# Optimization experiments

Hardware: AMD Instinct MI355X
Metric: run time of the kernel (lower is better)

The kernel has to match this reference:

```python
import jax, jax.numpy as jnp
import numpy as np

N_NODES = 100000

def gcn_conv(x, W, b, src, dst, n_nodes):
    # PyG GCNConv: out = D^{-1/2} (A + I) D^{-1/2} (x W) + b, deg includes self-loop
    h = x @ W  # [N, H]
    ones = jnp.ones(src.shape[0], dtype=x.dtype)
    deg = jax.ops.segment_sum(ones, dst, num_segments=n_nodes) + 1.0  # +1 self-loop
    dinv = jax.lax.rsqrt(deg)  # deg >= 1, no zeros
    norm = dinv[src] * dinv[dst]  # [E]
    msg = h[src] * norm[:, None]  # [E, H] gather + scale
    agg = jax.ops.segment_sum(msg, dst, num_segments=n_nodes)  # scatter-add
    self_contrib = h * (dinv * dinv)[:, None]  # self-loop term norm = dinv_i^2
    return agg + self_contrib + b


def setup_inputs() -> dict:
    key = jax.random.key(0)
    ks = jax.random.split(key, 6)
    F_IN, H, E = 128, 128, 1600000
    x = jax.random.normal(ks[0], (N_NODES, F_IN), dtype=jnp.float32)
    edge_index = jax.random.randint(ks[1], (2, E), 0, N_NODES, dtype=jnp.int32)
    s = 1.0 / np.sqrt(F_IN)
    W1 = jax.random.normal(ks[2], (F_IN, H), dtype=jnp.float32) * s
    b1 = jnp.zeros((H,), dtype=jnp.float32)
    W2 = jax.random.normal(ks[3], (H, H), dtype=jnp.float32) * (1.0 / np.sqrt(H))
    b2 = jnp.zeros((H,), dtype=jnp.float32)
    Wlin = jax.random.normal(ks[4], (H, 1), dtype=jnp.float32) * (1.0 / np.sqrt(H))
    blin = jnp.zeros((1,), dtype=jnp.float32)
    return {"x": x, "edge_index": edge_index, "W1": W1, "b1": b1,
            "W2": W2, "b2": b2, "Wlin": Wlin, "blin": blin}


def reference(x, edge_index, W1, b1, W2, b2, Wlin, blin):
    src, dst = edge_index[0], edge_index[1]
    h = gcn_conv(x, W1, b1, src, dst, N_NODES)
    h = jax.nn.relu(h)
    h = gcn_conv(h, W2, b2, src, dst, N_NODES)
    h = jax.nn.relu(h)
    out = h @ Wlin + blin  # [N, 1]
    return out.squeeze(-1)  # [N]
```

## Files before the change

kernel.cpp:

```cpp
#include <hip/hip_runtime.h>
#include <hip/hip_fp16.h>

#define NFEAT 128

typedef _Float16 v8hf __attribute__((ext_vector_type(8)));
typedef float v4f __attribute__((ext_vector_type(4)));

__global__ void k_deg_rank(const int* __restrict__ dst, int* __restrict__ deg,
                           int* __restrict__ rank, int E, int N) {
  int e = blockIdx.x * blockDim.x + threadIdx.x;
  if (e < E) rank[e] = atomicAdd(&deg[dst[e]], 1);
  else if (e < E + N) rank[e] = atomicAdd(&deg[e - E], 1);
}

__global__ void k_prep_w(const float* __restrict__ W1, const float* __restrict__ W2,
                         _Float16* __restrict__ Wt1, _Float16* __restrict__ Wt2) {
  int idx = blockIdx.x * 256 + threadIdx.x;
  const float* W = (idx < 16384) ? W1 : W2;
  _Float16* Wt = (idx < 16384) ? Wt1 : Wt2;
  int i = idx & 16383;
  int k = i >> 7, n = i & 127;
  Wt[n * 128 + k] = (_Float16)W[k * 128 + n];
}

__global__ __launch_bounds__(1024) void k_scan_blocks(const int* __restrict__ deg,
    int* __restrict__ base, int* __restrict__ partials, int n) {
  __shared__ int buf[1024];
  int tid = threadIdx.x;
  int i = blockIdx.x * 1024 + tid;
  int v = (i < n) ? deg[i] : 0;
  buf[tid] = v;
  __syncthreads();
  #pragma unroll
  for (int off = 1; off < 1024; off <<= 1) {
    int t = (tid >= off) ? buf[tid - off] : 0;
    __syncthreads();
    buf[tid] += t;
    __syncthreads();
  }
  if (i <= n) base[i] = buf[tid] - v;
  if (tid == 1023) partials[blockIdx.x] = buf[tid];
}

__global__ void k_scan_partials(int* __restrict__ partials, int nb) {
  __shared__ int buf[128];
  int tid = threadIdx.x;
  int v = (tid < nb) ? partials[tid] : 0;
  buf[tid] = v;
  __syncthreads();
  #pragma unroll
  for (int off = 1; off < 128; off <<= 1) {
    int t = (tid >= off) ? buf[tid - off] : 0;
    __syncthreads();
    buf[tid] += t;
    __syncthreads();
  }
  if (tid < nb) partials[tid] = buf[tid] - v;
}

__global__ void k_finalize_base(int* __restrict__ base, const int* __restrict__ partials,
    const int* __restrict__ deg, float* __restrict__ dinv, int n) {
  int i = blockIdx.x * blockDim.x + threadIdx.x;
  if (i <= n) {
    base[i] += partials[i >> 10];
    if (i < n) dinv[i] = rsqrtf((float)deg[i]);
  }
}

__global__ void k_scatter(const int* __restrict__ src, const int* __restrict__ dst,
    const int* __restrict__ rank, const int* __restrict__ base,
    int* __restrict__ ssrc, int E, int N) {
  int e = blockIdx.x * blockDim.x + threadIdx.x;
  if (e < E) ssrc[base[dst[e]] + rank[e]] = src[e];
  else if (e < E + N) { int n = e - E; ssrc[base[n] + rank[e]] = n; }
}

template <typename AT>
__global__ __launch_bounds__(256) void k_gemm_mfma(
    const AT* __restrict__ A, const _Float16* __restrict__ Wt,
    const float* __restrict__ dinv, _Float16* __restrict__ g16, int N) {
  __shared__ _Float16 As[64][136];
  __shared__ _Float16 Ws[128][136];
  const int tid = threadIdx.x;
  const int row0 = blockIdx.x * 64;

  if constexpr (sizeof(AT) == 4) {
    #pragma unroll
    for (int i = 0; i < 8; i++) {
      int idx = tid + i * 256;
      int row = idx >> 5;
      int c4 = idx & 31;
      int gr = row0 + row; gr = (gr < N) ? gr : (N - 1);
      float4 v = *(const float4*)((const float*)A + (size_t)gr * NFEAT + c4 * 4);
      _Float16* p = &As[row][c4 * 4];
      p[0] = (_Float16)v.x; p[1] = (_Float16)v.y;
      p[2] = (_Float16)v.z; p[3] = (_Float16)v.w;
    }
  } else {
    #pragma unroll
    for (int i = 0; i < 4; i++) {
      int idx = tid + i * 256;
      int row = idx >> 4;
      int c8 = idx & 15;
      int gr = row0 + row; gr = (gr < N) ? gr : (N - 1);
      *(uint4*)&As[row][c8 * 8] =
          *(const uint4*)((const _Float16*)A + (size_t)gr * NFEAT + c8 * 8);
    }
  }
  #pragma unroll
  for (int i = 0; i < 8; i++) {
    int idx = tid + i * 256;
    int row = idx >> 4;
    int c8 = idx & 15;
    *(uint4*)&Ws[row][c8 * 8] = *(const uint4*)(Wt + (size_t)row * 128 + c8 * 8);
  }
  __syncthreads();

  const int wv = tid >> 6;
  const int lane = tid & 63;
  const int m = lane & 15;
  const int q = lane >> 4;

  v4f acc[8] = {};
  const _Float16* arow = &As[wv * 16 + m][0];
  #pragma unroll
  for (int kt = 0; kt < 4; kt++) {
    v8hf af = *(const v8hf*)(arow + kt * 32 + q * 8);
    #pragma unroll
    for (int ct = 0; ct < 8; ct++) {
      v8hf bf = *(const v8hf*)(&Ws[ct * 16 + m][kt * 32 + q * 8]);
      acc[ct] = __builtin_amdgcn_mfma_f32_16x16x32_f16(af, bf, acc[ct], 0, 0, 0);
    }
  }

  int nd[4]; float dv[4];
  #pragma unroll
  for (int r = 0; r < 4; r++) {
    nd[r] = row0 + wv * 16 + q * 4 + r;
    int c = (nd[r] < N) ? nd[r] : (N - 1);
    dv[r] = dinv[c];
  }
  #pragma unroll
  for (int ct = 0; ct < 8; ct++)
    #pragma unroll
    for (int r = 0; r < 4; r++)
      if (nd[r] < N)
        g16[(size_t)nd[r] * NFEAT + ct * 16 + m] = (_Float16)(acc[ct][r] * dv[r]);
}

__global__ __launch_bounds__(256) void k_agg(
    const __half2* __restrict__ g, const float* __restrict__ dinv,
    const int* __restrict__ base, const int* __restrict__ ssrc,
    const float* __restrict__ bias, __half2* __restrict__ hB, int N) {
  const int lane = threadIdx.x & 63;
  const int n = blockIdx.x * 4 + (threadIdx.x >> 6);
  if (n >= N) return;
  int e = base[n], b1 = base[n + 1];
  float2 acc = make_float2(0.f, 0.f);
  for (; e + 8 <= b1; e += 8) {
    int s0 = ssrc[e],     s1 = ssrc[e + 1], s2 = ssrc[e + 2], s3 = ssrc[e + 3];
    int s4 = ssrc[e + 4], s5 = ssrc[e + 5], s6 = ssrc[e + 6], s7 = ssrc[e + 7];
    float2 f0 = __half22float2(g[(size_t)s0 * 64 + lane]);
    float2 f1 = __half22float2(g[(size_t)s1 * 64 + lane]);
    float2 f2 = __half22float2(g[(size_t)s2 * 64 + lane]);
    float2 f3 = __half22float2(g[(size_t)s3 * 64 + lane]);
    float2 f4 = __half22float2(g[(size_t)s4 * 64 + lane]);
    float2 f5 = __half22float2(g[(size_t)s5 * 64 + lane]);
    float2 f6 = __half22float2(g[(size_t)s6 * 64 + lane]);
    float2 f7 = __half22float2(g[(size_t)s7 * 64 + lane]);
    acc.x += (f0.x + f1.x) + (f2.x + f3.x) + (f4.x + f5.x) + (f6.x + f7.x);
    acc.y += (f0.y + f1.y) + (f2.y + f3.y) + (f4.y + f5.y) + (f6.y + f7.y);
  }
  for (; e < b1; ++e) {
    float2 f = __half22float2(g[(size_t)ssrc[e] * 64 + lane]);
    acc.x += f.x; acc.y += f.y;
  }
  float dvn = dinv[n];
  float2 bb = *(const float2*)(bias + lane * 2);
  hB[(size_t)n * 64 + lane] =
      __floats2half2_rn(fmaxf(acc.x * dvn + bb.x, 0.f),
                        fmaxf(acc.y * dvn + bb.y, 0.f));
}

__global__ __launch_bounds__(256) void k_agg_final(
    const __half2* __restrict__ g, const float* __restrict__ dinv,
    const int* __restrict__ base, const int* __restrict__ ssrc,
    const float* __restrict__ bias, const float* __restrict__ wlin,
    const float* __restrict__ blin, float* __restrict__ out, int N) {
  const int lane = threadIdx.x & 63;
  const int n = blockIdx.x * 4 + (threadIdx.x >> 6);
  if (n >= N) return;
  int e = base[n], b1 = base[n + 1];
  float2 acc = make_float2(0.f, 0.f);
  for (; e + 8 <= b1; e += 8) {
    int s0 = ssrc[e],     s1 = ssrc[e + 1], s2 = ssrc[e + 2], s3 = ssrc[e + 3];
    int s4 = ssrc[e + 4], s5 = ssrc[e + 5], s6 = ssrc[e + 6], s7 = ssrc[e + 7];
    float2 f0 = __half22float2(g[(size_t)s0 * 64 + lane]);
    float2 f1 = __half22float2(g[(size_t)s1 * 64 + lane]);
    float2 f2 = __half22float2(g[(size_t)s2 * 64 + lane]);
    float2 f3 = __half22float2(g[(size_t)s3 * 64 + lane]);
    float2 f4 = __half22float2(g[(size_t)s4 * 64 + lane]);
    float2 f5 = __half22float2(g[(size_t)s5 * 64 + lane]);
    float2 f6 = __half22float2(g[(size_t)s6 * 64 + lane]);
    float2 f7 = __half22float2(g[(size_t)s7 * 64 + lane]);
    acc.x += (f0.x + f1.x) + (f2.x + f3.x) + (f4.x + f5.x) + (f6.x + f7.x);
    acc.y += (f0.y + f1.y) + (f2.y + f3.y) + (f4.y + f5.y) + (f6.y + f7.y);
  }
  for (; e < b1; ++e) {
    float2 f = __half22float2(g[(size_t)ssrc[e] * 64 + lane]);
    acc.x += f.x; acc.y += f.y;
  }
  float dvn = dinv[n];
  float2 bb = *(const float2*)(bias + lane * 2);
  float2 wl = *(const float2*)(wlin + lane * 2);
  float pv = fmaxf(acc.x * dvn + bb.x, 0.f) * wl.x +
             fmaxf(acc.y * dvn + bb.y, 0.f) * wl.y;
  #pragma unroll
  for (int off = 32; off >= 1; off >>= 1) pv += __shfl_down(pv, off, 64);
  if (lane == 0) out[n] = pv + blin[0];
}

extern "C" void kernel_launch(void* const* d_in, const int* in_sizes, int n_in,
                              void* d_out, int out_size, void* d_ws, size_t ws_size,
                              hipStream_t stream) {
  const float* x    = (const float*)d_in[0];
  const int*   ei   = (const int*)d_in[1];
  const float* W1   = (const float*)d_in[2];
  const float* b1   = (const float*)d_in[3];
  const float* W2   = (const float*)d_in[4];
  const float* b2   = (const float*)d_in[5];
  const float* Wlin = (const float*)d_in[6];
  const float* blin = (const float*)d_in[7];
  const int N = in_sizes[0] / NFEAT;
  const int E = in_sizes[1] / 2;
  const int* src = ei;
  const int* dst = ei + E;
  const int Etot = E + N;

  int* ws_i = (int*)d_ws;
  size_t off = 0;
  int* deg      = ws_i + off; off += N;
  int* base     = ws_i + off; off += (size_t)N + 1;
  off = (off + 3) & ~(size_t)3;
  int* partials = ws_i + off; off += 128;
  int* ssrc     = ws_i + off; off += Etot;
  float* dinv   = (float*)(ws_i + off); off += N;
  off = (off + 3) & ~(size_t)3;
  _Float16* Wt1 = (_Float16*)(ws_i + off); off += 8192;
  _Float16* Wt2 = (_Float16*)(ws_i + off); off += 8192;
  _Float16* g16 = (_Float16*)(ws_i + off); off += (size_t)N * 64;
  _Float16* hB  = (_Float16*)(ws_i + off); off += (size_t)N * 64;
  int* rank     = (int*)g16;

  hipMemsetAsync(deg, 0, (size_t)N * sizeof(int), stream);

  const int tpbE = 256;
  const int gE = (Etot + tpbE - 1) / tpbE;
  k_deg_rank<<<gE, tpbE, 0, stream>>>(dst, deg, rank, E, N);
  k_prep_w<<<128, 256, 0, stream>>>(W1, W2, Wt1, Wt2);

  const int nb = (N + 1 + 1023) / 1024;
  k_scan_blocks<<<nb, 1024, 0, stream>>>(deg, base, partials, N);
  k_scan_partials<<<1, 128, 0, stream>>>(partials, nb);
  k_finalize_base<<<((N + 1) + 255) / 256, 256, 0, stream>>>(base, partials, deg, dinv, N);
  k_scatter<<<gE, tpbE, 0, stream>>>(src, dst, rank, base, ssrc, E, N);

  const int gg = (N + 63) / 64;
  const int ga = (N + 3) / 4;
  k_gemm_mfma<float><<<gg, 256, 0, stream>>>(x, Wt1, dinv, g16, N);
  k_agg<<<ga, 256, 0, stream>>>((const __half2*)g16, dinv, base, ssrc, b1,
                                (__half2*)hB, N);
  k_gemm_mfma<_Float16><<<gg, 256, 0, stream>>>(hB, Wt2, dinv, g16, N);
  k_agg_final<<<ga, 256, 0, stream>>>((const __half2*)g16, dinv, base, ssrc, b2,
                                      Wlin, blin, (float*)d_out, N);
}
```

Measured before the change: 401.2 us.

## Split wavefront into four edge groups with 16-byte vector gathers in aggregation

The aggregation kernels now split each 64-lane wavefront into four 16-lane groups. Each group gathers a whole 256-byte fp16 row with 16-byte vector loads, so one wave handles eight edges per iteration and partial sums are combined with cross-lane shuffles. Out-of-range edges are pointed at a zero padding row appended to the feature buffer, which removes the scalar tail loop. The weight-transpose kernel is also merged into the degree/rank kernel to save a launch. The cost is the extra shuffle reductions and some wasted loads on padded edges for low-degree nodes.

```diff
diff --git a/kernel.cpp b/kernel.cpp
--- a/kernel.cpp
+++ b/kernel.cpp
@@ -6,21 +6,21 @@
 typedef _Float16 v8hf __attribute__((ext_vector_type(8)));
 typedef float v4f __attribute__((ext_vector_type(4)));
 
-__global__ void k_deg_rank(const int* __restrict__ dst, int* __restrict__ deg,
-                           int* __restrict__ rank, int E, int N) {
+__global__ void k_deg_rank_w(const int* __restrict__ dst, int* __restrict__ deg,
+                             int* __restrict__ rank, int E, int N,
+                             const float* __restrict__ W1, const float* __restrict__ W2,
+                             _Float16* __restrict__ Wt1, _Float16* __restrict__ Wt2) {
   int e = blockIdx.x * blockDim.x + threadIdx.x;
   if (e < E) rank[e] = atomicAdd(&deg[dst[e]], 1);
   else if (e < E + N) rank[e] = atomicAdd(&deg[e - E], 1);
-}
-
-__global__ void k_prep_w(const float* __restrict__ W1, const float* __restrict__ W2,
-                         _Float16* __restrict__ Wt1, _Float16* __restrict__ Wt2) {
-  int idx = blockIdx.x * 256 + threadIdx.x;
-  const float* W = (idx < 16384) ? W1 : W2;
-  _Float16* Wt = (idx < 16384) ? Wt1 : Wt2;
-  int i = idx & 16383;
-  int k = i >> 7, n = i & 127;
-  Wt[n * 128 + k] = (_Float16)W[k * 128 + n];
+  else if (e < E + N + 32768) {
+    int idx = e - E - N;
+    const float* W = (idx < 16384) ? W1 : W2;
+    _Float16* Wt = (idx < 16384) ? Wt1 : Wt2;
+    int i = idx & 16383;
+    int k = i >> 7, n = i & 127;
+    Wt[n * 128 + k] = (_Float16)W[k * 128 + n];
+  }
 }
 
 __global__ __launch_bounds__(1024) void k_scan_blocks(const int* __restrict__ deg,
@@ -83,6 +83,13 @@
   __shared__ _Float16 Ws[128][136];
   const int tid = threadIdx.x;
   const int row0 = blockIdx.x * 64;
+
+  if (blockIdx.x == 0 && tid < 16) {
+    v8hf z;
+    #pragma unroll
+    for (int j = 0; j < 8; j++) z[j] = (_Float16)0.f;
+    *(v8hf*)(g16 + (size_t)N * NFEAT + tid * 8) = z;
+  }
 
   if constexpr (sizeof(AT) == 4) {
     #pragma unroll
@@ -149,74 +156,91 @@
 }
 
 __global__ __launch_bounds__(256) void k_agg(
-    const __half2* __restrict__ g, const float* __restrict__ dinv,
+    const _Float16* __restrict__ g, const float* __restrict__ dinv,
     const int* __restrict__ base, const int* __restrict__ ssrc,
-    const float* __restrict__ bias, __half2* __restrict__ hB, int N) {
+    const float* __restrict__ bias, _Float16* __restrict__ hB, int N) {
   const int lane = threadIdx.x & 63;
   const int n = blockIdx.x * 4 + (threadIdx.x >> 6);
   if (n >= N) return;
-  int e = base[n], b1 = base[n + 1];
-  float2 acc = make_float2(0.f, 0.f);
-  for (; e + 8 <= b1; e += 8) {
-    int s0 = ssrc[e],     s1 = ssrc[e + 1], s2 = ssrc[e + 2], s3 = ssrc[e + 3];
-    int s4 = ssrc[e + 4], s5 = ssrc[e + 5], s6 = ssrc[e + 6], s7 = ssrc[e + 7];
-    float2 f0 = __half22float2(g[(size_t)s0 * 64 + lane]);
-    float2 f1 = __half22float2(g[(size_t)s1 * 64 + lane]);
-    float2 f2 = __half22float2(g[(size_t)s2 * 64 + lane]);
-    float2 f3 = __half22float2(g[(size_t)s3 * 64 + lane]);
-    float2 f4 = __half22float2(g[(size_t)s4 * 64 + lane]);
-    float2 f5 = __half22float2(g[(size_t)s5 * 64 + lane]);
-    float2 f6 = __half22float2(g[(size_t)s6 * 64 + lane]);
-    float2 f7 = __half22float2(g[(size_t)s7 * 64 + lane]);
-    acc.x += (f0.x + f1.x) + (f2.x + f3.x) + (f4.x + f5.x) + (f6.x + f7.x);
-    acc.y += (f0.y + f1.y) + (f2.y + f3.y) + (f4.y + f5.y) + (f6.y + f7.y);
-  }
-  for (; e < b1; ++e) {
-    float2 f = __half22float2(g[(size_t)ssrc[e] * 64 + lane]);
-    acc.x += f.x; acc.y += f.y;
-  }
-  float dvn = dinv[n];
-  float2 bb = *(const float2*)(bias + lane * 2);
-  hB[(size_t)n * 64 + lane] =
-      __floats2half2_rn(fmaxf(acc.x * dvn + bb.x, 0.f),
-                        fmaxf(acc.y * dvn + bb.y, 0.f));
+  const int gq = lane >> 4;
+  const int l = lane & 15;
+  float acc[8] = {};
+  int b0 = base[n], b1 = base[n + 1];
+  for (int e = b0; e < b1; e += 8) {
+    int e0 = e + gq, e1 = e + 4 + gq;
+    int i0 = ssrc[e0];
+    int i1 = ssrc[e1];
+    i0 = (e0 < b1) ? i0 : N;
+    i1 = (e1 < b1) ? i1 : N;
+    v8hf r0 = *(const v8hf*)(g + (size_t)i0 * NFEAT + l * 8);
+    v8hf r1 = *(const v8hf*)(g + (size_t)i1 * NFEAT + l * 8);
+    #pragma unroll
+    for (int j = 0; j < 8; j++) acc[j] += (float)r0[j] + (float)r1[j];
+  }
+  #pragma unroll
+  for (int j = 0; j < 8; j++) {
+    acc[j] += __shfl_xor(acc[j], 16, 64);
+    acc[j] += __shfl_xor(acc[j], 32, 64);
+  }
+  if (gq == 0) {
+    float dvn = dinv[n];
+    const float* bp = bias + l * 8;
+    float4 bb0 = *(const float4*)(bp);
+    float4 bb1 = *(const float4*)(bp + 4);
+    float bv[8] = {bb0.x, bb0.y, bb0.z, bb0.w, bb1.x, bb1.y, bb1.z, bb1.w};
+    v8hf o;
+    #pragma unroll
+    for (int j = 0; j < 8; j++)
+      o[j] = (_Float16)fmaxf(acc[j] * dvn + bv[j], 0.f);
+    *(v8hf*)(hB + (size_t)n * NFEAT + l * 8) = o;
+  }
 }
 
 __global__ __launch_bounds__(256) void k_agg_final(
-    const __half2* __restrict__ g, const float* __restrict__ dinv,
+    const _Float16* __restrict__ g, const float* __restrict__ dinv,
     const int* __restrict__ base, const int* __restrict__ ssrc,
     const float* __restrict__ bias, const float* __restrict__ wlin,
     const float* __restrict__ blin, float* __restrict__ out, int N) {
   const int lane = threadIdx.x & 63;
   const int n = blockIdx.x * 4 + (threadIdx.x >> 6);
   if (n >= N) return;
-  int e = base[n], b1 = base[n + 1];
-  float2 acc = make_float2(0.f, 0.f);
-  for (; e + 8 <= b1; e += 8) {
-    int s0 = ssrc[e],     s1 = ssrc[e + 1], s2 = ssrc[e + 2], s3 = ssrc[e + 3];
-    int s4 = ssrc[e + 4], s5 = ssrc[e + 5], s6 = ssrc[e + 6], s7 = ssrc[e + 7];
-    float2 f0 = __half22float2(g[(size_t)s0 * 64 + lane]);
-    float2 f1 = __half22float2(g[(size_t)s1 * 64 + lane]);
-    float2 f2 = __half22float2(g[(size_t)s2 * 64 + lane]);
-    float2 f3 = __half22float2(g[(size_t)s3 * 64 + lane]);
-    float2 f4 = __half22float2(g[(size_t)s4 * 64 + lane]);
-    float2 f5 = __half22float2(g[(size_t)s5 * 64 + lane]);
-    float2 f6 = __half22float2(g[(size_t)s6 * 64 + lane]);
-    float2 f7 = __half22float2(g[(size_t)s7 * 64 + lane]);
-    acc.x += (f0.x + f1.x) + (f2.x + f3.x) + (f4.x + f5.x) + (f6.x + f7.x);
-    acc.y += (f0.y + f1.y) + (f2.y + f3.y) + (f4.y + f5.y) + (f6.y + f7.y);
-  }
-  for (; e < b1; ++e) {
-    float2 f = __half22float2(g[(size_t)ssrc[e] * 64 + lane]);
-    acc.x += f.x; acc.y += f.y;
+  const int gq = lane >> 4;
+  const int l = lane & 15;
+  float acc[8] = {};
+  int b0 = base[n], b1 = base[n + 1];
+  for (int e = b0; e < b1; e += 8) {
+    int e0 = e + gq, e1 = e + 4 + gq;
+    int i0 = ssrc[e0];
+    int i1 = ssrc[e1];
+    i0 = (e0 < b1) ? i0 : N;
+    i1 = (e1 < b1) ? i1 : N;
+    v8hf r0 = *(const v8hf*)(g + (size_t)i0 * NFEAT + l * 8);
+    v8hf r1 = *(const v8hf*)(g + (size_t)i1 * NFEAT + l * 8);
+    #pragma unroll
+    for (int j = 0; j < 8; j++) acc[j] += (float)r0[j] + (float)r1[j];
+  }
+  #pragma unroll
+  for (int j = 0; j < 8; j++) {
+    acc[j] += __shfl_xor(acc[j], 16, 64);
+    acc[j] += __shfl_xor(acc[j], 32, 64);
   }
   float dvn = dinv[n];
-  float2 bb = *(const float2*)(bias + lane * 2);
-  float2 wl = *(const float2*)(wlin + lane * 2);
-  float pv = fmaxf(acc.x * dvn + bb.x, 0.f) * wl.x +
-             fmaxf(acc.y * dvn + bb.y, 0.f) * wl.y;
-  #pragma unroll
-  for (int off = 32; off >= 1; off >>= 1) pv += __shfl_down(pv, off, 64);
+  const float* bp = bias + l * 8;
+  const float* wp = wlin + l * 8;
+  float4 bb0 = *(const float4*)(bp);
+  float4 bb1 = *(const float4*)(bp + 4);
+  float4 wl0 = *(const float4*)(wp);
+  float4 wl1 = *(const float4*)(wp + 4);
+  float bv[8] = {bb0.x, bb0.y, bb0.z, bb0.w, bb1.x, bb1.y, bb1.z, bb1.w};
+  float wv[8] = {wl0.x, wl0.y, wl0.z, wl0.w, wl1.x, wl1.y, wl1.z, wl1.w};
+  float pv = 0.f;
+  #pragma unroll
+  for (int j = 0; j < 8; j++)
+    pv += fmaxf(acc[j] * dvn + bv[j], 0.f) * wv[j];
+  pv += __shfl_xor(pv, 1, 64);
+  pv += __shfl_xor(pv, 2, 64);
+  pv += __shfl_xor(pv, 4, 64);
+  pv += __shfl_xor(pv, 8, 64);
   if (lane == 0) out[n] = pv + blin[0];
 }
 
@@ -243,34 +267,32 @@
   int* base     = ws_i + off; off += (size_t)N + 1;
   off = (off + 3) & ~(size_t)3;
   int* partials = ws_i + off; off += 128;
-  int* ssrc     = ws_i + off; off += Etot;
+  int* ssrc     = ws_i + off; off += Etot + 8;
   float* dinv   = (float*)(ws_i + off); off += N;
   off = (off + 3) & ~(size_t)3;
   _Float16* Wt1 = (_Float16*)(ws_i + off); off += 8192;
   _Float16* Wt2 = (_Float16*)(ws_i + off); off += 8192;
-  _Float16* g16 = (_Float16*)(ws_i + off); off += (size_t)N * 64;
+  _Float16* g16 = (_Float16*)(ws_i + off); off += (size_t)(N + 1) * 64;
   _Float16* hB  = (_Float16*)(ws_i + off); off += (size_t)N * 64;
   int* rank     = (int*)g16;
 
   hipMemsetAsync(deg, 0, (size_t)N * sizeof(int), stream);
 
   const int tpbE = 256;
-  const int gE = (Etot + tpbE - 1) / tpbE;
-  k_deg_rank<<<gE, tpbE, 0, stream>>>(dst, deg, rank, E, N);
-  k_prep_w<<<128, 256, 0, stream>>>(W1, W2, Wt1, Wt2);
+  const int gE = (Etot + 32768 + tpbE - 1) / tpbE;
+  k_deg_rank_w<<<gE, tpbE, 0, stream>>>(dst, deg, rank, E, N, W1, W2, Wt1, Wt2);
 
   const int nb = (N + 1 + 1023) / 1024;
   k_scan_blocks<<<nb, 1024, 0, stream>>>(deg, base, partials, N);
   k_scan_partials<<<1, 128, 0, stream>>>(partials, nb);
   k_finalize_base<<<((N + 1) + 255) / 256, 256, 0, stream>>>(base, partials, deg, dinv, N);
-  k_scatter<<<gE, tpbE, 0, stream>>>(src, dst, rank, base, ssrc, E, N);
+  k_scatter<<<(Etot + tpbE - 1) / tpbE, tpbE, 0, stream>>>(src, dst, rank, base, ssrc, E, N);
 
   const int gg = (N + 63) / 64;
   const int ga = (N + 3) / 4;
   k_gemm_mfma<float><<<gg, 256, 0, stream>>>(x, Wt1, dinv, g16, N);
-  k_agg<<<ga, 256, 0, stream>>>((const __half2*)g16, dinv, base, ssrc, b1,
-                                (__half2*)hB, N);
+  k_agg<<<ga, 256, 0, stream>>>(g16, dinv, base, ssrc, b1, hB, N);
   k_gemm_mfma<_Float16><<<gg, 256, 0, stream>>>(hB, Wt2, dinv, g16, N);
-  k_agg_final<<<ga, 256, 0, stream>>>((const __half2*)g16, dinv, base, ssrc, b2,
+  k_agg_final<<<ga, 256, 0, stream>>>(g16, dinv, base, ssrc, b2,
                                       Wlin, blin, (float*)d_out, N);
 }
```

Measured after the change: 386.9 us. -3.6%, faster.
